# Optimization experiments

Hardware: AMD Instinct MI355X
Metric: run time of the kernel (lower is better)

Reference implementation:

```python
import jax, jax.numpy as jnp
import numpy as np

D_MODEL = 1024
D_FF = 2048
N_EXPERTS = 8
TOP_K = 2


def setup_inputs() -> dict:
    key = jax.random.key(0)
    ks = jax.random.split(key, 10)
    s = 0.02
    return {
        "x": jax.random.normal(ks[0], (2, 1024, D_MODEL), dtype=jnp.float32),
        "gate_w": jax.random.normal(ks[1], (N_EXPERTS, D_MODEL), dtype=jnp.float32) * s,
        "gate_b": jnp.zeros((N_EXPERTS,), jnp.float32),
        "Wg": jax.random.normal(ks[2], (N_EXPERTS, D_MODEL, D_FF), dtype=jnp.float32) * s,
        "bg": jnp.zeros((N_EXPERTS, D_FF), jnp.float32),
        "Wu": jax.random.normal(ks[3], (N_EXPERTS, D_MODEL, D_FF), dtype=jnp.float32) * s,
        "bu": jnp.zeros((N_EXPERTS, D_FF), jnp.float32),
        "Wd": jax.random.normal(ks[4], (N_EXPERTS, D_FF, D_MODEL), dtype=jnp.float32) * s,
        "bd": jnp.zeros((N_EXPERTS, D_MODEL), jnp.float32),
    }


def reference(x, gate_w, gate_b, Wg, bg, Wu, bu, Wd, bd):
    b, s, d = x.shape
    xf = x.reshape(-1, d)                       # (T, d)
    T = xf.shape[0]
    # --- router ---
    logits = xf @ gate_w.T + gate_b             # (T, E)
    probs = jax.nn.softmax(logits.astype(jnp.float32), axis=-1)
    # load-balance loss: KL(ideal || mean_probs), reduction='sum'
    expert_probs = probs.mean(axis=0)
    ideal = 1.0 / N_EXPERTS
    balance_loss = jnp.sum(ideal * (jnp.log(ideal) - jnp.log(expert_probs + 1e-9)))
    # top-k routing, renormalized
    vals, idx = jax.lax.top_k(probs, TOP_K)     # (T, K)
    w = vals / vals.sum(axis=-1, keepdims=True)
    # per-token per-expert combine weight (T, E); zero for non-selected experts
    cw = jnp.zeros((T, N_EXPERTS), jnp.float32).at[
        jnp.arange(T)[:, None], idx].add(w)
    # --- experts (SwiGLU MLP), batched over E, masked combine ---
    g = jnp.einsum('td,edf->tef', xf, Wg) + bg[None]   # (T, E, F)
    u = jnp.einsum('td,edf->tef', xf, Wu) + bu[None]
    h = jax.nn.silu(g) * u
    out = jnp.einsum('tef,efd->ted', h, Wd) + bd[None]  # (T, E, d)
    y = jnp.einsum('ted,te->td', out, cw.astype(x.dtype))
    return y.reshape(b, s, d), balance_loss
```

## Files before the change

kernel.cpp:

```cpp
#include <hip/hip_runtime.h>
#include <hip/hip_bf16.h>


#define D_MODEL 1024
#define D_FF    2048
#define N_EXP   8
#define T_TOK   2048
#define MAXTILES 40

typedef __attribute__((ext_vector_type(8))) short bf16x8;
typedef __attribute__((ext_vector_type(8))) ushort u16x8;
typedef __attribute__((ext_vector_type(4))) float f32x4;

__device__ __forceinline__ ushort f2bf(float f) {
    union { float f; unsigned u; } c; c.f = f;
    unsigned u = c.u;
    return (ushort)((u + 0x7fffu + ((u >> 16) & 1u)) >> 16);
}

__device__ __forceinline__ void glds16(const void* g, void* l) {
    __builtin_amdgcn_global_load_lds(
        (const __attribute__((address_space(1))) unsigned int*)g,
        (__attribute__((address_space(3))) unsigned int*)l, 16, 0, 0);
}

__global__ void k_convert_x(const float* __restrict__ x, ushort* __restrict__ xb) {
    int idx = blockIdx.x * 256 + threadIdx.x;
    float4 v = ((const float4*)x)[idx];
    ushort4 o;
    o.x = f2bf(v.x); o.y = f2bf(v.y); o.z = f2bf(v.z); o.w = f2bf(v.w);
    ((ushort4*)xb)[idx] = o;
}

__global__ __launch_bounds__(256) void k_prep_w(
    const float* __restrict__ Wg, const float* __restrict__ Wu, const float* __restrict__ Wd,
    ushort* __restrict__ Wgt, ushort* __restrict__ Wut, ushort* __restrict__ Wdt)
{
    int t = blockIdx.x;
    int which = blockIdx.y;
    const float* src; ushort* dst; int N, K, nt, kt;
    int e = t >> 8;
    if (which == 2) { src = Wd; dst = Wdt; N = 1024; K = 2048; nt = (t >> 5) & 7;  kt = t & 31; }
    else            { src = (which ? Wu : Wg); dst = (which ? Wut : Wgt); N = 2048; K = 1024; nt = (t >> 4) & 15; kt = t & 15; }

    int tid = threadIdx.x;
    int ncol = tid & 127, kbh = (tid >> 7) * 4;
    const float* colp = src + (size_t)e * K * N + (size_t)(kt * 64) * N + nt * 128 + ncol;
    ushort* dtile = dst + (size_t)t * 8192;
#pragma unroll
    for (int i = 0; i < 4; i++) {
        int kb = kbh + i;
        const float* p = colp + (size_t)(kb * 8) * N;
        u16x8 o;
#pragma unroll
        for (int j = 0; j < 8; j++) o[j] = f2bf(p[(size_t)j * N]);
        *(u16x8*)&dtile[(kb * 128 + ncol) * 8] = o;
    }
}

__global__ __launch_bounds__(256) void k_router(
    const float* __restrict__ x, const float* __restrict__ gw, const float* __restrict__ gb,
    int* cnt, float* probsum, int* tok, int* slotpk, float* wtok)
{
    __shared__ float gws[N_EXP * D_MODEL];
    __shared__ float ps_s[N_EXP];
    __shared__ int   bc_s[N_EXP];
    __shared__ int   gb_s[N_EXP];
    __shared__ int   a_e[64];
    __shared__ int   a_lp[64];

    int tid = threadIdx.x;
    for (int i = tid; i < N_EXP * D_MODEL / 4; i += 256)
        ((float4*)gws)[i] = ((const float4*)gw)[i];
    if (tid < N_EXP) { ps_s[tid] = 0.f; bc_s[tid] = 0; }
    __syncthreads();

    int wave = tid >> 6, lane = tid & 63;

    for (int it = 0; it < 8; it++) {
        int tb = it * 4 + wave;
        int t = blockIdx.x * 32 + tb;
        const float4* xr = (const float4*)(x + (size_t)t * D_MODEL);

        float acc[N_EXP];
#pragma unroll
        for (int e = 0; e < N_EXP; e++) acc[e] = 0.f;
#pragma unroll
        for (int q = 0; q < 4; q++) {
            int idx = q * 64 + lane;
            float4 xv = xr[idx];
#pragma unroll
            for (int e = 0; e < N_EXP; e++) {
                float4 gv = ((const float4*)(gws + e * D_MODEL))[idx];
                acc[e] += xv.x * gv.x + xv.y * gv.y + xv.z * gv.z + xv.w * gv.w;
            }
        }
#pragma unroll
        for (int off = 32; off > 0; off >>= 1) {
#pragma unroll
            for (int e = 0; e < N_EXP; e++) acc[e] += __shfl_xor(acc[e], off, 64);
        }
        if (lane == 0) {
            float l[N_EXP], m = -1e30f;
#pragma unroll
            for (int e = 0; e < N_EXP; e++) { l[e] = acc[e] + gb[e]; m = fmaxf(m, l[e]); }
            float p[N_EXP], s = 0.f;
#pragma unroll
            for (int e = 0; e < N_EXP; e++) { p[e] = expf(l[e] - m); s += p[e]; }
            float inv = 1.f / s;
#pragma unroll
            for (int e = 0; e < N_EXP; e++) { p[e] *= inv; atomicAdd(&ps_s[e], p[e]); }
            int i0 = 0; float v0 = p[0];
#pragma unroll
            for (int e = 1; e < N_EXP; e++) if (p[e] > v0) { v0 = p[e]; i0 = e; }
            int i1 = -1; float v1 = -1.f;
#pragma unroll
            for (int e = 0; e < N_EXP; e++) if (e != i0 && p[e] > v1) { v1 = p[e]; i1 = e; }
            float winv = 1.f / (v0 + v1);
            int lp0 = atomicAdd(&bc_s[i0], 1);
            int lp1 = atomicAdd(&bc_s[i1], 1);
            a_e[tb * 2 + 0] = i0; a_lp[tb * 2 + 0] = lp0;
            a_e[tb * 2 + 1] = i1; a_lp[tb * 2 + 1] = lp1;
            wtok[t * 2 + 0] = v0 * winv;
            wtok[t * 2 + 1] = v1 * winv;
        }
    }
    __syncthreads();
    if (tid < N_EXP) {
        gb_s[tid] = atomicAdd(&cnt[tid], bc_s[tid]);
        atomicAdd(&probsum[tid], ps_s[tid]);
    }
    __syncthreads();
    if (tid < 64) {
        int tb = tid >> 1, k = tid & 1;
        int t = blockIdx.x * 32 + tb;
        int e = a_e[tid];
        int slot = gb_s[e] + a_lp[tid];
        tok[e * T_TOK + slot] = t;
        slotpk[t * 2 + k] = (e << 16) | slot;
    }
}

__global__ void k_base_loss(const int* __restrict__ cnt, const float* __restrict__ probsum,
                            int* abase, int* tile, float* loss_out)
{
    if (threadIdx.x == 0 && blockIdx.x == 0) {
        int b = 0, nt = 0;
        float loss = 0.f;
        for (int e = 0; e < N_EXP; e++) {
            abase[e] = b;
            for (int m0 = 0; m0 < cnt[e]; m0 += 128)
                tile[nt++] = (e << 16) | m0;
            b += ((cnt[e] + 127) >> 7) * 128;
            float mean = probsum[e] * (1.0f / T_TOK);
            loss += 0.125f * (logf(0.125f) - logf(mean + 1e-9f));
        }
        for (; nt < MAXTILES; nt++) tile[nt] = -1;
        *loss_out = loss;
    }
}

__global__ __launch_bounds__(256, 2) void k_expert_gu(
    const ushort* __restrict__ Wgt, const ushort* __restrict__ Wut,
    const float* __restrict__ bg, const float* __restrict__ bu,
    const ushort* __restrict__ xb, const int* __restrict__ cnt,
    const int* __restrict__ abase, const int* __restrict__ tile,
    const int* __restrict__ tok, ushort* __restrict__ h_t)
{
    int ti = tile[blockIdx.x];
    if (ti < 0) return;
    int e = ti >> 16, m0 = ti & 0xffff;
    int ne = cnt[e];
    int nt = blockIdx.y;
    int n0 = nt * 128;
    int stile = (abase[e] >> 7) + (m0 >> 7);

    __shared__ __align__(16) ushort As[128 * 88];
    __shared__ __align__(16) ushort Bg_s[8192];
    __shared__ __align__(16) ushort Bu_s[8192];

    int tid = threadIdx.x;
    int lane = tid & 63, wave = tid >> 6;
    int wm = (wave & 1) * 64, wn = (wave >> 1) * 64;

    int arow = tid >> 1;
    int akh = (tid & 1) * 32;
    int atok = tok[e * T_TOK + min(m0 + arow, ne - 1)];
    const ushort* xrow = xb + (size_t)atok * D_MODEL;

    const char* gbase = (const char*)(Wgt + (size_t)(e * 16 + nt) * 16 * 8192);
    const char* ubase = (const char*)(Wut + (size_t)(e * 16 + nt) * 16 * 8192);
    int goff = tid * 16;
    int loff = (tid >> 6) * 1024;

    f32x4 accg[4][4], accu[4][4];
#pragma unroll
    for (int i = 0; i < 4; i++)
#pragma unroll
        for (int j = 0; j < 4; j++) {
            accg[i][j] = (f32x4){0.f, 0.f, 0.f, 0.f};
            accu[i][j] = (f32x4){0.f, 0.f, 0.f, 0.f};
        }

    for (int kt = 0; kt < D_MODEL / 64; kt++) {
        __syncthreads();
#pragma unroll
        for (int q = 0; q < 4; q++)
            *(uint4*)&As[arow * 88 + akh + q * 8] = *(const uint4*)&xrow[kt * 64 + akh + q * 8];
        const char* gsrc = gbase + kt * 16384;
        const char* usrc = ubase + kt * 16384;
#pragma unroll
        for (int q = 0; q < 4; q++) {
            glds16(gsrc + q * 4096 + goff, (char*)Bg_s + q * 4096 + loff);
            glds16(usrc + q * 4096 + goff, (char*)Bu_s + q * 4096 + loff);
        }
        __syncthreads();
#pragma unroll
        for (int ks = 0; ks < 2; ks++) {
            bf16x8 af[4];
            int arow_f = wm + (lane & 15);
            int akb = ks * 32 + (lane >> 4) * 8;
#pragma unroll
            for (int sm = 0; sm < 4; sm++)
                af[sm] = *(const bf16x8*)&As[(arow_f + sm * 16) * 88 + akb];
            int bkb = ks * 4 + (lane >> 4);
#pragma unroll
            for (int sn = 0; sn < 4; sn++) {
                int ncol = wn + sn * 16 + (lane & 15);
                bf16x8 bgf = *(const bf16x8*)&Bg_s[(bkb * 128 + ncol) * 8];
                bf16x8 buf = *(const bf16x8*)&Bu_s[(bkb * 128 + ncol) * 8];
#pragma unroll
                for (int sm = 0; sm < 4; sm++) {
                    accg[sm][sn] = __builtin_amdgcn_mfma_f32_16x16x32_bf16(af[sm], bgf, accg[sm][sn], 0, 0, 0);
                    accu[sm][sn] = __builtin_amdgcn_mfma_f32_16x16x32_bf16(af[sm], buf, accu[sm][sn], 0, 0, 0);
                }
            }
        }
    }
    int rbase = wm + ((lane >> 4) << 2);
    int cbase = wn + (lane & 15);
    size_t tbase = (size_t)stile * 32 * 8192;
#pragma unroll
    for (int sm = 0; sm < 4; sm++) {
#pragma unroll
        for (int r = 0; r < 4; r++) {
            int pos = m0 + rbase + sm * 16 + r;
            if (pos < ne) {
                int row = pos & 127;
#pragma unroll
                for (int sn = 0; sn < 4; sn++) {
                    int col = n0 + cbase + sn * 16;
                    float g = accg[sm][sn][r] + bg[e * D_FF + col];
                    float u = accu[sm][sn][r] + bu[e * D_FF + col];
                    float hv = (g / (1.f + expf(-g))) * u;
                    int ktb = col >> 6, kb = (col >> 3) & 7, ko = col & 7;
                    h_t[tbase + (size_t)ktb * 8192 + (kb * 128 + row) * 8 + ko] = f2bf(hv);
                }
            }
        }
    }
}

__global__ __launch_bounds__(256, 2) void k_expert_down(
    const ushort* __restrict__ Wdt, const float* __restrict__ bd,
    const ushort* __restrict__ h_t, const int* __restrict__ cnt,
    const int* __restrict__ abase, const int* __restrict__ tile,
    float* __restrict__ outp)
{
    int ti = tile[blockIdx.x];
    if (ti < 0) return;
    int e = ti >> 16, m0 = ti & 0xffff;
    int ne = cnt[e];
    int nt = blockIdx.y;
    int n0 = nt * 128;
    int stile = (abase[e] >> 7) + (m0 >> 7);

    __shared__ __align__(16) ushort As8[8192];
    __shared__ __align__(16) ushort Bd_s[8192];

    int tid = threadIdx.x;
    int lane = tid & 63, wave = tid >> 6;
    int wm = (wave & 1) * 64, wn = (wave >> 1) * 64;

    const char* hbase = (const char*)(h_t + (size_t)stile * 32 * 8192);
    const char* dbase = (const char*)(Wdt + (size_t)(e * 8 + nt) * 32 * 8192);
    int goff = tid * 16;
    int loff = (tid >> 6) * 1024;

    f32x4 acc[4][4];
#pragma unroll
    for (int i = 0; i < 4; i++)
#pragma unroll
        for (int j = 0; j < 4; j++) acc[i][j] = (f32x4){0.f, 0.f, 0.f, 0.f};

    for (int kt = 0; kt < D_FF / 64; kt++) {
        __syncthreads();
        const char* asrc = hbase + kt * 16384;
        const char* bsrc = dbase + kt * 16384;
#pragma unroll
        for (int q = 0; q < 4; q++) {
            glds16(asrc + q * 4096 + goff, (char*)As8 + q * 4096 + loff);
            glds16(bsrc + q * 4096 + goff, (char*)Bd_s + q * 4096 + loff);
        }
        __syncthreads();
#pragma unroll
        for (int ks = 0; ks < 2; ks++) {
            bf16x8 af[4];
            int kb = ks * 4 + (lane >> 4);
            int arow_f = wm + (lane & 15);
#pragma unroll
            for (int sm = 0; sm < 4; sm++)
                af[sm] = *(const bf16x8*)&As8[(kb * 128 + arow_f + sm * 16) * 8];
#pragma unroll
            for (int sn = 0; sn < 4; sn++) {
                int ncol = wn + sn * 16 + (lane & 15);
                bf16x8 bdf = *(const bf16x8*)&Bd_s[(kb * 128 + ncol) * 8];
#pragma unroll
                for (int sm = 0; sm < 4; sm++)
                    acc[sm][sn] = __builtin_amdgcn_mfma_f32_16x16x32_bf16(af[sm], bdf, acc[sm][sn], 0, 0, 0);
            }
        }
    }
    int rbase = wm + ((lane >> 4) << 2);
    int cbase = wn + (lane & 15);
#pragma unroll
    for (int sm = 0; sm < 4; sm++) {
#pragma unroll
        for (int r = 0; r < 4; r++) {
            int pos = m0 + rbase + sm * 16 + r;
            if (pos < ne) {
                size_t ob = (size_t)(abase[e] + pos) * D_MODEL;
#pragma unroll
                for (int sn = 0; sn < 4; sn++) {
                    int col = n0 + cbase + sn * 16;
                    outp[ob + col] = acc[sm][sn][r] + bd[e * D_MODEL + col];
                }
            }
        }
    }
}

__global__ void k_combine(const float* __restrict__ outp, const int* __restrict__ slotpk,
                          const float* __restrict__ wtok, const int* __restrict__ abase,
                          float* __restrict__ y)
{
    int idx = blockIdx.x * 256 + threadIdx.x;
    int t = idx >> 8, j = idx & 255;
    int sp0 = slotpk[t * 2 + 0], sp1 = slotpk[t * 2 + 1];
    float w0 = wtok[t * 2 + 0], w1 = wtok[t * 2 + 1];
    size_t s0 = (size_t)abase[sp0 >> 16] + (sp0 & 0xffff);
    size_t s1 = (size_t)abase[sp1 >> 16] + (sp1 & 0xffff);
    float4 a = ((const float4*)outp)[s0 * (D_MODEL / 4) + j];
    float4 b = ((const float4*)outp)[s1 * (D_MODEL / 4) + j];
    float4 o;
    o.x = w0 * a.x + w1 * b.x;
    o.y = w0 * a.y + w1 * b.y;
    o.z = w0 * a.z + w1 * b.z;
    o.w = w0 * a.w + w1 * b.w;
    ((float4*)y)[idx] = o;
}

extern "C" void kernel_launch(void* const* d_in, const int* in_sizes, int n_in,
                              void* d_out, int out_size, void* d_ws, size_t ws_size,
                              hipStream_t stream)
{
    const float* x  = (const float*)d_in[0];
    const float* gw = (const float*)d_in[1];
    const float* gb = (const float*)d_in[2];
    const float* Wg = (const float*)d_in[3];
    const float* bg = (const float*)d_in[4];
    const float* Wu = (const float*)d_in[5];
    const float* bu = (const float*)d_in[6];
    const float* Wd = (const float*)d_in[7];
    const float* bd = (const float*)d_in[8];
    float* y = (float*)d_out;
    float* loss_out = y + (size_t)T_TOK * D_MODEL;

    char* ws = (char*)d_ws;
    int*    cnt     = (int*)(ws + 0);
    float*  probsum = (float*)(ws + 128);
    int*    abase   = (int*)(ws + 256);
    int*    tiletab = (int*)(ws + 320);
    int*    slotpk  = (int*)(ws + 512);
    float*  wtok    = (float*)(ws + 16896);
    int*    tok     = (int*)(ws + 33280);
    ushort* xb      = (ushort*)(ws + 131072);
    ushort* Wgt     = (ushort*)(ws + 4325376);
    ushort* Wut     = (ushort*)(ws + 37879808);
    ushort* Wdt     = (ushort*)(ws + 71434240);
    ushort* h_t     = (ushort*)(ws + 104988672);
    float*  outp    = (float*)(ws + 125960192);

    hipMemsetAsync(d_ws, 0, 256, stream);
    k_prep_w<<<dim3(2048, 3), dim3(256), 0, stream>>>(Wg, Wu, Wd, Wgt, Wut, Wdt);
    k_convert_x<<<dim3(2048), dim3(256), 0, stream>>>(x, xb);
    k_router<<<dim3(64), dim3(256), 0, stream>>>(x, gw, gb, cnt, probsum, tok, slotpk, wtok);
    k_base_loss<<<dim3(1), dim3(64), 0, stream>>>(cnt, probsum, abase, tiletab, loss_out);
    k_expert_gu<<<dim3(MAXTILES, 16), dim3(256), 0, stream>>>(Wgt, Wut, bg, bu, xb, cnt, abase, tiletab, tok, h_t);
    k_expert_down<<<dim3(MAXTILES, 8), dim3(256), 0, stream>>>(Wdt, bd, h_t, cnt, abase, tiletab, outp);
    k_combine<<<dim3(2048), dim3(256), 0, stream>>>(outp, slotpk, wtok, abase, y);
}
```

Measured before the change: 398.7 us.

## Coalesce weight prep via LDS, fuse x conversion into router, atomic combine

Weight conversion now stages rows into LDS with async global-to-LDS loads so each thread reads contiguous floats, replacing the strided column reads of the old prep kernel. The x-to-bf16 conversion moves into the router, which already reads x, so x is read only once. The combine kernel and the fp32 expert-output buffer are removed: the down-projection scatters weighted results into y with atomic adds after a memset of y. The atomics make the summation order nondeterministic and add contention when two experts update the same token row.

Result: slower. 526.0 us (+31.9%).

```diff
diff --git a/kernel.cpp b/kernel.cpp
--- a/kernel.cpp
+++ b/kernel.cpp
@@ -24,43 +24,104 @@
         (__attribute__((address_space(3))) unsigned int*)l, 16, 0, 0);
 }
 
-__global__ void k_convert_x(const float* __restrict__ x, ushort* __restrict__ xb) {
-    int idx = blockIdx.x * 256 + threadIdx.x;
-    float4 v = ((const float4*)x)[idx];
-    ushort4 o;
-    o.x = f2bf(v.x); o.y = f2bf(v.y); o.z = f2bf(v.z); o.w = f2bf(v.w);
-    ((ushort4*)xb)[idx] = o;
-}
-
 __global__ __launch_bounds__(256) void k_prep_w(
     const float* __restrict__ Wg, const float* __restrict__ Wu, const float* __restrict__ Wd,
     ushort* __restrict__ Wgt, ushort* __restrict__ Wut, ushort* __restrict__ Wdt)
 {
-    int t = blockIdx.x;
-    int which = blockIdx.y;
-    const float* src; ushort* dst; int N, K, nt, kt;
-    int e = t >> 8;
-    if (which == 2) { src = Wd; dst = Wdt; N = 1024; K = 2048; nt = (t >> 5) & 7;  kt = t & 31; }
-    else            { src = (which ? Wu : Wg); dst = (which ? Wut : Wgt); N = 2048; K = 1024; nt = (t >> 4) & 15; kt = t & 15; }
-
-    int tid = threadIdx.x;
-    int ncol = tid & 127, kbh = (tid >> 7) * 4;
-    const float* colp = src + (size_t)e * K * N + (size_t)(kt * 64) * N + nt * 128 + ncol;
-    ushort* dtile = dst + (size_t)t * 8192;
-#pragma unroll
-    for (int i = 0; i < 4; i++) {
-        int kb = kbh + i;
-        const float* p = colp + (size_t)(kb * 8) * N;
-        u16x8 o;
-#pragma unroll
-        for (int j = 0; j < 8; j++) o[j] = f2bf(p[(size_t)j * N]);
-        *(u16x8*)&dtile[(kb * 128 + ncol) * 8] = o;
+    __shared__ __align__(16) float lds[8224];
+    int tid = threadIdx.x, lane = tid & 63, w = tid >> 6;
+    int x = blockIdx.x;
+
+    if (blockIdx.y == 0) {
+        int which = x >> 7;
+        int e = (x >> 4) & 7, kt = x & 15;
+        const float* src = (which ? Wu : Wg) + ((size_t)e * 1024 + kt * 64) * 2048;
+        ushort* dst = which ? Wut : Wgt;
+        const int S = 2052;
+        int lp = ((lane & 3) << 4) | (lane >> 2);
+        int n = (w * 64 + lp) * 8;
+        int nt = n >> 7, nl = n & 127;
+        ushort* dt = dst + (((size_t)(e * 16 + nt)) * 16 + kt) * 8192 + nl * 8;
+
+        for (int c = 0; c < 16; c++) {
+            __syncthreads();
+            const float* rp = src + (size_t)(c * 4 + w) * 2048;
+            float* lr = lds + w * S;
+#pragma unroll
+            for (int s = 0; s < 8; s++)
+                glds16(rp + s * 256 + lane * 4, lr + s * 256 + lane * 4);
+            __syncthreads();
+
+            float4 v[4][2];
+#pragma unroll
+            for (int i = 0; i < 4; i++) {
+                int r = ((lane & 3) + i) & 3;
+                const float4* p = (const float4*)(lds + r * S + n);
+                v[r][0] = p[0]; v[r][1] = p[1];
+            }
+            float el[4][8];
+#pragma unroll
+            for (int r = 0; r < 4; r++) {
+                el[r][0] = v[r][0].x; el[r][1] = v[r][0].y; el[r][2] = v[r][0].z; el[r][3] = v[r][0].w;
+                el[r][4] = v[r][1].x; el[r][5] = v[r][1].y; el[r][6] = v[r][1].z; el[r][7] = v[r][1].w;
+            }
+            int kb = c >> 1, koh = (c & 1) * 4;
+            ushort* dd = dt + kb * 1024 + koh;
+#pragma unroll
+            for (int j = 0; j < 8; j++) {
+                ushort4 o;
+                o.x = f2bf(el[0][j]); o.y = f2bf(el[1][j]);
+                o.z = f2bf(el[2][j]); o.w = f2bf(el[3][j]);
+                *(ushort4*)(dd + j * 8) = o;
+            }
+        }
+    } else {
+        int e = x >> 5, kt = x & 31;
+        const float* src = Wd + ((size_t)e * 2048 + kt * 64) * 1024;
+        const int S = 1028;
+        int lp = ((lane & 7) << 3) | (lane >> 3);
+        int n = (w * 64 + lp) * 4;
+        int nt = n >> 7, nl = n & 127;
+        ushort* dt = Wdt + (((size_t)(e * 8 + nt)) * 32 + kt) * 8192 + nl * 8;
+
+        for (int c = 0; c < 8; c++) {
+            __syncthreads();
+            const float* rp = src + (size_t)(c * 8 + w * 2) * 1024;
+#pragma unroll
+            for (int s = 0; s < 4; s++) {
+                glds16(rp + s * 256 + lane * 4,        lds + (w * 2) * S + s * 256 + lane * 4);
+                glds16(rp + 1024 + s * 256 + lane * 4, lds + (w * 2 + 1) * S + s * 256 + lane * 4);
+            }
+            __syncthreads();
+
+            float4 v[8];
+#pragma unroll
+            for (int i = 0; i < 8; i++) {
+                int r = ((lane & 7) + i) & 7;
+                v[r] = *(const float4*)(lds + r * S + n);
+            }
+            ushort* dd = dt + c * 1024;
+#pragma unroll
+            for (int j = 0; j < 4; j++) {
+                u16x8 o;
+                o[0] = f2bf(j == 0 ? v[0].x : j == 1 ? v[0].y : j == 2 ? v[0].z : v[0].w);
+                o[1] = f2bf(j == 0 ? v[1].x : j == 1 ? v[1].y : j == 2 ? v[1].z : v[1].w);
+                o[2] = f2bf(j == 0 ? v[2].x : j == 1 ? v[2].y : j == 2 ? v[2].z : v[2].w);
+                o[3] = f2bf(j == 0 ? v[3].x : j == 1 ? v[3].y : j == 2 ? v[3].z : v[3].w);
+                o[4] = f2bf(j == 0 ? v[4].x : j == 1 ? v[4].y : j == 2 ? v[4].z : v[4].w);
+                o[5] = f2bf(j == 0 ? v[5].x : j == 1 ? v[5].y : j == 2 ? v[5].z : v[5].w);
+                o[6] = f2bf(j == 0 ? v[6].x : j == 1 ? v[6].y : j == 2 ? v[6].z : v[6].w);
+                o[7] = f2bf(j == 0 ? v[7].x : j == 1 ? v[7].y : j == 2 ? v[7].z : v[7].w);
+                *(u16x8*)(dd + j * 8) = o;
+            }
+        }
     }
 }
 
 __global__ __launch_bounds__(256) void k_router(
     const float* __restrict__ x, const float* __restrict__ gw, const float* __restrict__ gb,
-    int* cnt, float* probsum, int* tok, int* slotpk, float* wtok)
+    int* cnt, float* probsum, int* tok, float* wslot,
+    ushort* __restrict__ xb)
 {
     __shared__ float gws[N_EXP * D_MODEL];
     __shared__ float ps_s[N_EXP];
@@ -68,6 +129,7 @@
     __shared__ int   gb_s[N_EXP];
     __shared__ int   a_e[64];
     __shared__ int   a_lp[64];
+    __shared__ float a_w[64];
 
     int tid = threadIdx.x;
     for (int i = tid; i < N_EXP * D_MODEL / 4; i += 256)
@@ -81,6 +143,7 @@
         int tb = it * 4 + wave;
         int t = blockIdx.x * 32 + tb;
         const float4* xr = (const float4*)(x + (size_t)t * D_MODEL);
+        ushort* xbr = xb + (size_t)t * D_MODEL;
 
         float acc[N_EXP];
 #pragma unroll
@@ -89,6 +152,9 @@
         for (int q = 0; q < 4; q++) {
             int idx = q * 64 + lane;
             float4 xv = xr[idx];
+            ushort4 xc;
+            xc.x = f2bf(xv.x); xc.y = f2bf(xv.y); xc.z = f2bf(xv.z); xc.w = f2bf(xv.w);
+            *(ushort4*)&xbr[idx * 4] = xc;
 #pragma unroll
             for (int e = 0; e < N_EXP; e++) {
                 float4 gv = ((const float4*)(gws + e * D_MODEL))[idx];
@@ -119,10 +185,8 @@
             float winv = 1.f / (v0 + v1);
             int lp0 = atomicAdd(&bc_s[i0], 1);
             int lp1 = atomicAdd(&bc_s[i1], 1);
-            a_e[tb * 2 + 0] = i0; a_lp[tb * 2 + 0] = lp0;
-            a_e[tb * 2 + 1] = i1; a_lp[tb * 2 + 1] = lp1;
-            wtok[t * 2 + 0] = v0 * winv;
-            wtok[t * 2 + 1] = v1 * winv;
+            a_e[tb * 2 + 0] = i0; a_lp[tb * 2 + 0] = lp0; a_w[tb * 2 + 0] = v0 * winv;
+            a_e[tb * 2 + 1] = i1; a_lp[tb * 2 + 1] = lp1; a_w[tb * 2 + 1] = v1 * winv;
         }
     }
     __syncthreads();
@@ -132,12 +196,12 @@
     }
     __syncthreads();
     if (tid < 64) {
-        int tb = tid >> 1, k = tid & 1;
+        int tb = tid >> 1;
         int t = blockIdx.x * 32 + tb;
         int e = a_e[tid];
         int slot = gb_s[e] + a_lp[tid];
         tok[e * T_TOK + slot] = t;
-        slotpk[t * 2 + k] = (e << 16) | slot;
+        wslot[e * T_TOK + slot] = a_w[tid];
     }
 }
 
@@ -265,7 +329,8 @@
     const ushort* __restrict__ Wdt, const float* __restrict__ bd,
     const ushort* __restrict__ h_t, const int* __restrict__ cnt,
     const int* __restrict__ abase, const int* __restrict__ tile,
-    float* __restrict__ outp)
+    const int* __restrict__ tok, const float* __restrict__ wslot,
+    float* __restrict__ y)
 {
     int ti = tile[blockIdx.x];
     if (ti < 0) return;
@@ -329,35 +394,17 @@
         for (int r = 0; r < 4; r++) {
             int pos = m0 + rbase + sm * 16 + r;
             if (pos < ne) {
-                size_t ob = (size_t)(abase[e] + pos) * D_MODEL;
+                int t = tok[e * T_TOK + pos];
+                float wgt = wslot[e * T_TOK + pos];
+                float* yrow = y + (size_t)t * D_MODEL;
 #pragma unroll
                 for (int sn = 0; sn < 4; sn++) {
                     int col = n0 + cbase + sn * 16;
-                    outp[ob + col] = acc[sm][sn][r] + bd[e * D_MODEL + col];
+                    atomicAdd(&yrow[col], wgt * (acc[sm][sn][r] + bd[e * D_MODEL + col]));
                 }
             }
         }
     }
-}
-
-__global__ void k_combine(const float* __restrict__ outp, const int* __restrict__ slotpk,
-                          const float* __restrict__ wtok, const int* __restrict__ abase,
-                          float* __restrict__ y)
-{
-    int idx = blockIdx.x * 256 + threadIdx.x;
-    int t = idx >> 8, j = idx & 255;
-    int sp0 = slotpk[t * 2 + 0], sp1 = slotpk[t * 2 + 1];
-    float w0 = wtok[t * 2 + 0], w1 = wtok[t * 2 + 1];
-    size_t s0 = (size_t)abase[sp0 >> 16] + (sp0 & 0xffff);
-    size_t s1 = (size_t)abase[sp1 >> 16] + (sp1 & 0xffff);
-    float4 a = ((const float4*)outp)[s0 * (D_MODEL / 4) + j];
-    float4 b = ((const float4*)outp)[s1 * (D_MODEL / 4) + j];
-    float4 o;
-    o.x = w0 * a.x + w1 * b.x;
-    o.y = w0 * a.y + w1 * b.y;
-    o.z = w0 * a.z + w1 * b.z;
-    o.w = w0 * a.w + w1 * b.w;
-    ((float4*)y)[idx] = o;
 }
 
 extern "C" void kernel_launch(void* const* d_in, const int* in_sizes, int n_in,
@@ -381,22 +428,19 @@
     float*  probsum = (float*)(ws + 128);
     int*    abase   = (int*)(ws + 256);
     int*    tiletab = (int*)(ws + 320);
-    int*    slotpk  = (int*)(ws + 512);
-    float*  wtok    = (float*)(ws + 16896);
-    int*    tok     = (int*)(ws + 33280);
+    float*  wslot   = (float*)(ws + 512);
+    int*    tok     = (int*)(ws + 66048);
     ushort* xb      = (ushort*)(ws + 131072);
     ushort* Wgt     = (ushort*)(ws + 4325376);
     ushort* Wut     = (ushort*)(ws + 37879808);
     ushort* Wdt     = (ushort*)(ws + 71434240);
     ushort* h_t     = (ushort*)(ws + 104988672);
-    float*  outp    = (float*)(ws + 125960192);
 
     hipMemsetAsync(d_ws, 0, 256, stream);
-    k_prep_w<<<dim3(2048, 3), dim3(256), 0, stream>>>(Wg, Wu, Wd, Wgt, Wut, Wdt);
-    k_convert_x<<<dim3(2048), dim3(256), 0, stream>>>(x, xb);
-    k_router<<<dim3(64), dim3(256), 0, stream>>>(x, gw, gb, cnt, probsum, tok, slotpk, wtok);
+    hipMemsetAsync(d_out, 0, (size_t)T_TOK * D_MODEL * sizeof(float), stream);
+    k_prep_w<<<dim3(256, 2), dim3(256), 0, stream>>>(Wg, Wu, Wd, Wgt, Wut, Wdt);
+    k_router<<<dim3(64), dim3(256), 0, stream>>>(x, gw, gb, cnt, probsum, tok, wslot, xb);
     k_base_loss<<<dim3(1), dim3(64), 0, stream>>>(cnt, probsum, abase, tiletab, loss_out);
     k_expert_gu<<<dim3(MAXTILES, 16), dim3(256), 0, stream>>>(Wgt, Wut, bg, bu, xb, cnt, abase, tiletab, tok, h_t);
-    k_expert_down<<<dim3(MAXTILES, 8), dim3(256), 0, stream>>>(Wdt, bd, h_t, cnt, abase, tiletab, outp);
-    k_combine<<<dim3(2048), dim3(256), 0, stream>>>(outp, slotpk, wtok, abase, y);
-}
+    k_expert_down<<<dim3(MAXTILES, 8), dim3(256), 0, stream>>>(Wdt, bd, h_t, cnt, abase, tiletab, tok, wslot, y);
+}
```
